# Optimization experiments

Measured on AMD Instinct MI355X. Metric: run time of the kernel, lower is better.

## Reference

```python
import jax, jax.numpy as jnp
import numpy as np

N_NODES = 50000
N_EDGES = 800000
F_IN = 64
F_HID = 64
F_OUT = 16


def setup_inputs() -> dict:
    key = jax.random.key(0)
    k1, k2, k3, k4, k5 = jax.random.split(key, 5)
    x = jax.random.normal(k1, (N_NODES, F_IN), dtype=jnp.float32)
    edge_index = jax.random.randint(k2, (2, N_EDGES), 0, N_NODES, dtype=jnp.int64)
    # glorot-style init for GCNConv weights
    W1 = jax.random.normal(k3, (F_IN, F_HID), dtype=jnp.float32) * (1.0 / np.sqrt(F_IN))
    b1 = jnp.zeros((F_HID,), dtype=jnp.float32)
    W2 = jax.random.normal(k4, (F_HID, F_OUT), dtype=jnp.float32) * (1.0 / np.sqrt(F_HID))
    b2 = jnp.zeros((F_OUT,), dtype=jnp.float32)
    return {"x": x, "edge_index": edge_index, "W1": W1, "b1": b1, "W2": W2, "b2": b2}


def _gcn_conv(x, src, dst, n, W, b):
    # linear transform first (PyG GCNConv), then normalized scatter-add aggregation
    h = x @ W  # [N, F_out]
    deg = jax.ops.segment_sum(jnp.ones_like(dst, dtype=h.dtype), dst, num_segments=n)
    dinv = jnp.where(deg > 0, jax.lax.rsqrt(deg), 0.0)  # deg^{-1/2}, 0 for isolated
    norm = dinv[src] * dinv[dst]  # [E]
    out = jax.ops.segment_sum(norm[:, None] * h[src], dst, num_segments=n)
    return out + b


def reference(x, edge_index, W1, b1, W2, b2):
    n = x.shape[0]
    loops = jnp.arange(n, dtype=edge_index.dtype)
    # add self-loops as in PyG GCNConv default
    src = jnp.concatenate([edge_index[0], loops])
    dst = jnp.concatenate([edge_index[1], loops])
    h = jax.nn.relu(_gcn_conv(x, src, dst, n, W1, b1))
    h = _gcn_conv(h, src, dst, n, W2, b2)
    return jax.nn.log_softmax(h, axis=1)
```

## Files before the change

### kernel.cpp

```cpp
#include <hip/hip_runtime.h>


#define F1 64
#define F2 16
#define G 256
#define HP 512

typedef __attribute__((ext_vector_type(8))) short bf16x8;
typedef __attribute__((ext_vector_type(4))) float f32x4;

__device__ inline void cvt8(const float* v, bf16x8& h, bf16x8& l) {
#pragma unroll
    for (int i = 0; i < 8; ++i) {
        unsigned b = __float_as_uint(v[i]);
        h[i] = (short)(b >> 16);
        float hif = __uint_as_float(b & 0xFFFF0000u);
        float lof = v[i] - hif;
        l[i] = (short)(__float_as_uint(lof) >> 16);
    }
}


__global__ __launch_bounds__(256) void k_hist(const int* __restrict__ dst,
                                              int* __restrict__ hist,
                                              int* __restrict__ ptotal,
                                              int e, int npart) {
    __shared__ int hl[HP];
    int tid = threadIdx.x, g = blockIdx.x;
    for (int i = tid; i < HP; i += 256) hl[i] = 0;
    __syncthreads();
    int chunk = (e + G - 1) / G;
    int beg = g * chunk, end = min(e, beg + chunk);
    for (int i = beg + tid; i < end; i += 256)
        atomicAdd(&hl[dst[i] >> 7], 1);
    __syncthreads();
    for (int p = tid; p < npart; p += 256) {
        int v = hl[p];
        hist[g * HP + p] = v;
        if (v) atomicAdd(&ptotal[p], v);
    }
}

__global__ __launch_bounds__(512) void k_pscan(const int* __restrict__ ptotal,
                                               int* __restrict__ part_base,
                                               int* __restrict__ rowstart,
                                               int npart, int n, int e) {
    __shared__ int s[512];
    int tid = threadIdx.x;
    int v = (tid < npart) ? ptotal[tid] : 0;
    s[tid] = v;
    __syncthreads();
    for (int off = 1; off < 512; off <<= 1) {
        int t = (tid >= off) ? s[tid - off] : 0;
        __syncthreads();
        s[tid] += t;
        __syncthreads();
    }
    if (tid < npart) part_base[tid] = s[tid] - v;
    if (tid == 0) { part_base[npart] = e; rowstart[n] = e; }
}

__global__ __launch_bounds__(256) void k_cscan(const int* __restrict__ hist,
                                               const int* __restrict__ part_base,
                                               int* __restrict__ pgoff, int npart) {
    __shared__ int s[G];
    int p = blockIdx.x, g = threadIdx.x;
    int v = hist[g * HP + p];
    s[g] = v;
    __syncthreads();
    for (int off = 1; off < G; off <<= 1) {
        int t = (g >= off) ? s[g - off] : 0;
        __syncthreads();
        s[g] += t;
        __syncthreads();
    }
    pgoff[g * HP + p] = part_base[p] + s[g] - v;
}

__global__ __launch_bounds__(256) void k_part(const int* __restrict__ src,
                                              const int* __restrict__ dst,
                                              const int* __restrict__ pgoff,
                                              unsigned* __restrict__ pairs,
                                              int e, int npart) {
    __shared__ int cur[HP];
    int tid = threadIdx.x, g = blockIdx.x;
    for (int i = tid; i < npart; i += 256) cur[i] = pgoff[g * HP + i];
    __syncthreads();
    int chunk = (e + G - 1) / G;
    int beg = g * chunk, end = min(e, beg + chunk);
    for (int i = beg + tid; i < end; i += 256) {
        int d = dst[i], sv = src[i];
        int pos = atomicAdd(&cur[d >> 7], 1);
        pairs[pos] = ((unsigned)(d & 127) << 16) | (unsigned)sv;
    }
}

__global__ __launch_bounds__(256) void k_csr(const unsigned* __restrict__ pairs,
                                             const int* __restrict__ part_base,
                                             int* __restrict__ rowstart,
                                             float* __restrict__ dinv,
                                             int* __restrict__ csr, int n) {
    __shared__ int cnt[128], cur[128], sc[128];
    int p = blockIdx.x, tid = threadIdx.x;
    int wbeg = part_base[p], wend = part_base[p + 1];
    if (tid < 128) cnt[tid] = 0;
    __syncthreads();
    for (int i = wbeg + tid; i < wend; i += 256)
        atomicAdd(&cnt[pairs[i] >> 16], 1);
    __syncthreads();
    if (tid < 128) sc[tid] = cnt[tid];
    __syncthreads();
    for (int off = 1; off < 128; off <<= 1) {
        int t = (tid >= off && tid < 128) ? sc[tid - off] : 0;
        __syncthreads();
        if (tid < 128) sc[tid] += t;
        __syncthreads();
    }
    if (tid < 128) {
        int v = cnt[tid];
        int rs = wbeg + sc[tid] - v;
        cur[tid] = rs;
        int node = (p << 7) + tid;
        if (node < n) {
            rowstart[node] = rs;
            dinv[node] = rsqrtf((float)v + 1.0f);
        }
    }
    __syncthreads();
    for (int i = wbeg + tid; i < wend; i += 256) {
        unsigned u = pairs[i];
        int pos = atomicAdd(&cur[u >> 16], 1);
        csr[pos] = (int)(u & 0xFFFFu);
    }
}


__global__ __launch_bounds__(256) void k_mgemm1(const float* __restrict__ x,
                                                const float* __restrict__ W1,
                                                float* __restrict__ h, int n) {
    __shared__ float ws[64 * 65];
    int tid = threadIdx.x;
    for (int i = tid; i < 64 * 64; i += 256) {
        int k = i >> 6, c = i & 63;
        ws[k * 65 + c] = W1[i];
    }
    __syncthreads();
    int lane = tid & 63, wv = tid >> 6;
    int rt = blockIdx.x * 64 + wv * 16;
    int r = lane & 15, g = lane >> 4;
    int row = rt + r;
    int rowc = row < n ? row : n - 1;
    const float* xp = x + (size_t)rowc * F1 + g * 8;
    bf16x8 ah[2], al[2];
#pragma unroll
    for (int kb = 0; kb < 2; ++kb) {
        float v[8];
        *(float4*)&v[0] = *(const float4*)(xp + kb * 32);
        *(float4*)&v[4] = *(const float4*)(xp + kb * 32 + 4);
        cvt8(v, ah[kb], al[kb]);
    }
#pragma unroll
    for (int ct = 0; ct < 4; ++ct) {
        bf16x8 bh[2], bl[2];
#pragma unroll
        for (int kb = 0; kb < 2; ++kb) {
            float v[8];
#pragma unroll
            for (int i = 0; i < 8; ++i)
                v[i] = ws[(kb * 32 + g * 8 + i) * 65 + ct * 16 + r];
            cvt8(v, bh[kb], bl[kb]);
        }
        f32x4 acc = {0.f, 0.f, 0.f, 0.f};
#pragma unroll
        for (int kb = 0; kb < 2; ++kb) {
            acc = __builtin_amdgcn_mfma_f32_16x16x32_bf16(ah[kb], bh[kb], acc, 0, 0, 0);
            acc = __builtin_amdgcn_mfma_f32_16x16x32_bf16(al[kb], bh[kb], acc, 0, 0, 0);
            acc = __builtin_amdgcn_mfma_f32_16x16x32_bf16(ah[kb], bl[kb], acc, 0, 0, 0);
        }
#pragma unroll
        for (int j = 0; j < 4; ++j) {
            int orow = rt + g * 4 + j;
            if (orow < n) h[(size_t)orow * F1 + ct * 16 + r] = acc[j];
        }
    }
}

__global__ __launch_bounds__(256) void k_mgemm2(const float* __restrict__ agg1,
                                                const float* __restrict__ b1,
                                                const float* __restrict__ W2,
                                                float* __restrict__ h2, int n) {
    __shared__ float ws[64 * 17];
    int tid = threadIdx.x;
    for (int i = tid; i < 64 * 16; i += 256) {
        int k = i >> 4, c = i & 15;
        ws[k * 17 + c] = W2[i];
    }
    __syncthreads();
    int lane = tid & 63, wv = tid >> 6;
    int rt = blockIdx.x * 64 + wv * 16;
    int r = lane & 15, g = lane >> 4;
    int row = rt + r;
    int rowc = row < n ? row : n - 1;
    const float* ap = agg1 + (size_t)rowc * F1 + g * 8;
    const float* bp = b1 + g * 8;
    bf16x8 ah[2], al[2];
#pragma unroll
    for (int kb = 0; kb < 2; ++kb) {
        float v[8], b[8];
        *(float4*)&v[0] = *(const float4*)(ap + kb * 32);
        *(float4*)&v[4] = *(const float4*)(ap + kb * 32 + 4);
        *(float4*)&b[0] = *(const float4*)(bp + kb * 32);
        *(float4*)&b[4] = *(const float4*)(bp + kb * 32 + 4);
#pragma unroll
        for (int i = 0; i < 8; ++i) v[i] = fmaxf(v[i] + b[i], 0.f);
        cvt8(v, ah[kb], al[kb]);
    }
    bf16x8 bh[2], bl[2];
#pragma unroll
    for (int kb = 0; kb < 2; ++kb) {
        float v[8];
#pragma unroll
        for (int i = 0; i < 8; ++i)
            v[i] = ws[(kb * 32 + g * 8 + i) * 17 + r];
        cvt8(v, bh[kb], bl[kb]);
    }
    f32x4 acc = {0.f, 0.f, 0.f, 0.f};
#pragma unroll
    for (int kb = 0; kb < 2; ++kb) {
        acc = __builtin_amdgcn_mfma_f32_16x16x32_bf16(ah[kb], bh[kb], acc, 0, 0, 0);
        acc = __builtin_amdgcn_mfma_f32_16x16x32_bf16(al[kb], bh[kb], acc, 0, 0, 0);
        acc = __builtin_amdgcn_mfma_f32_16x16x32_bf16(ah[kb], bl[kb], acc, 0, 0, 0);
    }
#pragma unroll
    for (int j = 0; j < 4; ++j) {
        int orow = rt + g * 4 + j;
        if (orow < n) h2[(size_t)orow * F2 + r] = acc[j];
    }
}


__global__ __launch_bounds__(256) void k_agg64(const int* __restrict__ rowstart,
                                               const int* __restrict__ csr,
                                               const float* __restrict__ dinv,
                                               const float* __restrict__ h,
                                               float* __restrict__ agg, int n) {
    int lane = threadIdx.x & 63, wv = threadIdx.x >> 6;
    int node = blockIdx.x * 4 + wv;
    if (node >= n) return;
    int g = lane >> 4, q = lane & 15;
    float di = dinv[node];
    const float4* h4 = (const float4*)h;
    float4 acc = {0.f, 0.f, 0.f, 0.f};
    int beg = rowstart[node], end = rowstart[node + 1];
    for (int base = beg; base < end; base += 64) {
        int k = base + lane;
        int idx = (k < end) ? csr[k] : 0;
        float dv = (k < end) ? dinv[idx] : 0.0f;
        int m = end - base;
        if (m > 64) m = 64;
        int iters = (m + 3) >> 2;
        for (int i = 0; i < iters; ++i) {
            int slot = i * 4 + g;
            int s = __shfl(idx, slot, 64);
            float w = __shfl(dv, slot, 64);
            float4 v = h4[(size_t)s * 16 + q];
            acc.x = fmaf(w, v.x, acc.x);
            acc.y = fmaf(w, v.y, acc.y);
            acc.z = fmaf(w, v.z, acc.z);
            acc.w = fmaf(w, v.w, acc.w);
        }
    }
#pragma unroll
    for (int off = 16; off <= 32; off <<= 1) {
        acc.x += __shfl_xor(acc.x, off, 64);
        acc.y += __shfl_xor(acc.y, off, 64);
        acc.z += __shfl_xor(acc.z, off, 64);
        acc.w += __shfl_xor(acc.w, off, 64);
    }
    if (g == 0) {
        float4 sv = h4[(size_t)node * 16 + q];
        float d2 = di * di;
        float4 o;
        o.x = fmaf(di, acc.x, d2 * sv.x);
        o.y = fmaf(di, acc.y, d2 * sv.y);
        o.z = fmaf(di, acc.z, d2 * sv.z);
        o.w = fmaf(di, acc.w, d2 * sv.w);
        ((float4*)agg)[(size_t)node * 16 + q] = o;
    }
}

__global__ __launch_bounds__(256) void k_agg16(const int* __restrict__ rowstart,
                                               const int* __restrict__ csr,
                                               const float* __restrict__ dinv,
                                               const float* __restrict__ h2,
                                               const float* __restrict__ b2,
                                               float* __restrict__ out, int n) {
    int lane = threadIdx.x & 63, wv = threadIdx.x >> 6;
    int node = blockIdx.x * 4 + wv;
    if (node >= n) return;
    int g = lane >> 2, q = lane & 3;
    float di = dinv[node];
    const float4* h4 = (const float4*)h2;
    float4 acc = {0.f, 0.f, 0.f, 0.f};
    int beg = rowstart[node], end = rowstart[node + 1];
    for (int base = beg; base < end; base += 64) {
        int k = base + lane;
        int idx = (k < end) ? csr[k] : 0;
        float dv = (k < end) ? dinv[idx] : 0.0f;
        int m = end - base;
        if (m > 64) m = 64;
        int iters = (m + 15) >> 4;
        for (int i = 0; i < iters; ++i) {
            int slot = i * 16 + g;
            int s = __shfl(idx, slot, 64);
            float w = __shfl(dv, slot, 64);
            float4 v = h4[(size_t)s * 4 + q];
            acc.x = fmaf(w, v.x, acc.x);
            acc.y = fmaf(w, v.y, acc.y);
            acc.z = fmaf(w, v.z, acc.z);
            acc.w = fmaf(w, v.w, acc.w);
        }
    }
#pragma unroll
    for (int off = 4; off <= 32; off <<= 1) {
        acc.x += __shfl_xor(acc.x, off, 64);
        acc.y += __shfl_xor(acc.y, off, 64);
        acc.z += __shfl_xor(acc.z, off, 64);
        acc.w += __shfl_xor(acc.w, off, 64);
    }
    float4 sv = h4[(size_t)node * 4 + q];
    float4 bv = ((const float4*)b2)[q];
    float d2 = di * di;
    float4 v;
    v.x = fmaf(di, acc.x, fmaf(d2, sv.x, bv.x));
    v.y = fmaf(di, acc.y, fmaf(d2, sv.y, bv.y));
    v.z = fmaf(di, acc.z, fmaf(d2, sv.z, bv.z));
    v.w = fmaf(di, acc.w, fmaf(d2, sv.w, bv.w));
    float mr = fmaxf(fmaxf(v.x, v.y), fmaxf(v.z, v.w));
    mr = fmaxf(mr, __shfl_xor(mr, 1, 64));
    mr = fmaxf(mr, __shfl_xor(mr, 2, 64));
    float s = expf(v.x - mr) + expf(v.y - mr) + expf(v.z - mr) + expf(v.w - mr);
    s += __shfl_xor(s, 1, 64);
    s += __shfl_xor(s, 2, 64);
    float l = mr + logf(s);
    if (g == 0) {
        float4 o;
        o.x = v.x - l; o.y = v.y - l; o.z = v.z - l; o.w = v.w - l;
        ((float4*)out)[(size_t)node * 4 + q] = o;
    }
}

extern "C" void kernel_launch(void* const* d_in, const int* in_sizes, int n_in,
                              void* d_out, int out_size, void* d_ws, size_t ws_size,
                              hipStream_t stream) {
    const float* x  = (const float*)d_in[0];
    const int*   ei = (const int*)d_in[1];
    const float* W1 = (const float*)d_in[2];
    const float* b1 = (const float*)d_in[3];
    const float* W2 = (const float*)d_in[4];
    const float* b2 = (const float*)d_in[5];
    float* out = (float*)d_out;

    const int n = in_sizes[0] / F1;
    const int e = in_sizes[1] / 2;
    const int* src = ei;
    const int* dst = ei + e;

    const int na = (n + 63) & ~63;
    const int npart = (n + 127) >> 7;

    float* dinv     = (float*)d_ws;
    int* rowstart   = (int*)(dinv + na);
    int* part_base  = rowstart + na + 64;
    int* ptotal     = part_base + 576;
    int* csr        = ptotal + 512;
    float* h        = (float*)(csr + ((e + 63) & ~63));
    float* agg1     = h + (size_t)n * F1;
    int* hist       = (int*)h;
    int* pgoff      = hist + G * HP;
    unsigned* pairs = (unsigned*)(pgoff + G * HP);

    hipMemsetAsync(ptotal, 0, HP * sizeof(int), stream);
    k_hist <<<G, 256, 0, stream>>>(dst, hist, ptotal, e, npart);
    k_pscan<<<1, 512, 0, stream>>>(ptotal, part_base, rowstart, npart, n, e);
    k_cscan<<<npart, 256, 0, stream>>>(hist, part_base, pgoff, npart);
    k_part <<<G, 256, 0, stream>>>(src, dst, pgoff, pairs, e, npart);
    k_csr  <<<npart, 256, 0, stream>>>(pairs, part_base, rowstart, dinv, csr, n);

    k_mgemm1<<<(n + 63) / 64, 256, 0, stream>>>(x, W1, h, n);
    k_agg64<<<(n + 3) / 4, 256, 0, stream>>>(rowstart, csr, dinv, h, agg1, n);

    float* h2 = h;
    k_mgemm2<<<(n + 63) / 64, 256, 0, stream>>>(agg1, b1, W2, h2, n);
    k_agg16<<<(n + 3) / 4, 256, 0, stream>>>(rowstart, csr, dinv, h2, b2, out, n);
}
```

Measured before the change: 171.2 us.

## Store GEMM outputs in bf16 and simplify CSR build to fewer kernels

Both GEMM stages now write their outputs as bf16 instead of fp32, halving the gather traffic in the two aggregation kernels. The CSR construction widens partitions to 256 nodes, drops the memset and the single-block prefix-scan kernel by recomputing partition bases redundantly in each block, and vectorises the edge reads with int4 loads. This removes two launches and some serial work, but the bf16 storage lowers the precision of the gathered features. Packing the source index into 16 bits assumes node ids fit that field (50000 does).

```diff
diff --git a/kernel.cpp b/kernel.cpp
--- a/kernel.cpp
+++ b/kernel.cpp
@@ -4,10 +4,19 @@
 #define F1 64
 #define F2 16
 #define G 256
-#define HP 512
+#define HP 256
 
 typedef __attribute__((ext_vector_type(8))) short bf16x8;
 typedef __attribute__((ext_vector_type(4))) float f32x4;
+typedef __attribute__((ext_vector_type(4))) unsigned short u16x4;
+
+__device__ inline unsigned short f2bf(float f) {
+    unsigned u = __float_as_uint(f);
+    return (unsigned short)((u + 0x7FFFu + ((u >> 16) & 1u)) >> 16);
+}
+__device__ inline float bf2f(unsigned short s) {
+    return __uint_as_float(((unsigned)s) << 16);
+}
 
 __device__ inline void cvt8(const float* v, bf16x8& h, bf16x8& l) {
 #pragma unroll
@@ -21,48 +30,31 @@
 }
 
 
-__global__ __launch_bounds__(256) void k_hist(const int* __restrict__ dst,
-                                              int* __restrict__ hist,
-                                              int* __restrict__ ptotal,
-                                              int e, int npart) {
+__global__ __launch_bounds__(256) void k_hist(const int4* __restrict__ dst4,
+                                              const int* __restrict__ dst,
+                                              int* __restrict__ hist, int e4, int e) {
     __shared__ int hl[HP];
     int tid = threadIdx.x, g = blockIdx.x;
-    for (int i = tid; i < HP; i += 256) hl[i] = 0;
-    __syncthreads();
-    int chunk = (e + G - 1) / G;
-    int beg = g * chunk, end = min(e, beg + chunk);
-    for (int i = beg + tid; i < end; i += 256)
-        atomicAdd(&hl[dst[i] >> 7], 1);
-    __syncthreads();
-    for (int p = tid; p < npart; p += 256) {
-        int v = hl[p];
-        hist[g * HP + p] = v;
-        if (v) atomicAdd(&ptotal[p], v);
-    }
-}
-
-__global__ __launch_bounds__(512) void k_pscan(const int* __restrict__ ptotal,
-                                               int* __restrict__ part_base,
-                                               int* __restrict__ rowstart,
-                                               int npart, int n, int e) {
-    __shared__ int s[512];
-    int tid = threadIdx.x;
-    int v = (tid < npart) ? ptotal[tid] : 0;
-    s[tid] = v;
-    __syncthreads();
-    for (int off = 1; off < 512; off <<= 1) {
-        int t = (tid >= off) ? s[tid - off] : 0;
-        __syncthreads();
-        s[tid] += t;
-        __syncthreads();
-    }
-    if (tid < npart) part_base[tid] = s[tid] - v;
-    if (tid == 0) { part_base[npart] = e; rowstart[n] = e; }
+    hl[tid] = 0;
+    __syncthreads();
+    int chunk = (e4 + G - 1) / G;
+    int beg = g * chunk, end = min(e4, beg + chunk);
+    for (int i = beg + tid; i < end; i += 256) {
+        int4 d = dst4[i];
+        atomicAdd(&hl[d.x >> 8], 1);
+        atomicAdd(&hl[d.y >> 8], 1);
+        atomicAdd(&hl[d.z >> 8], 1);
+        atomicAdd(&hl[d.w >> 8], 1);
+    }
+    if (g == G - 1)
+        for (int i = e4 * 4 + tid; i < e; i += 256) atomicAdd(&hl[dst[i] >> 8], 1);
+    __syncthreads();
+    hist[g * HP + tid] = hl[tid];
 }
 
 __global__ __launch_bounds__(256) void k_cscan(const int* __restrict__ hist,
-                                               const int* __restrict__ part_base,
-                                               int* __restrict__ pgoff, int npart) {
+                                               int* __restrict__ pgoff,
+                                               int* __restrict__ ptotal) {
     __shared__ int s[G];
     int p = blockIdx.x, g = threadIdx.x;
     int v = hist[g * HP + p];
@@ -74,58 +66,94 @@
         s[g] += t;
         __syncthreads();
     }
-    pgoff[g * HP + p] = part_base[p] + s[g] - v;
-}
-
-__global__ __launch_bounds__(256) void k_part(const int* __restrict__ src,
+    pgoff[g * HP + p] = s[g] - v;
+    if (g == G - 1) ptotal[p] = s[g];
+}
+
+__global__ __launch_bounds__(256) void k_part(const int4* __restrict__ src4,
+                                              const int4* __restrict__ dst4,
+                                              const int* __restrict__ src,
                                               const int* __restrict__ dst,
                                               const int* __restrict__ pgoff,
+                                              const int* __restrict__ ptotal,
                                               unsigned* __restrict__ pairs,
-                                              int e, int npart) {
+                                              int e4, int e, int npart) {
+    __shared__ int s[HP];
     __shared__ int cur[HP];
     int tid = threadIdx.x, g = blockIdx.x;
-    for (int i = tid; i < npart; i += 256) cur[i] = pgoff[g * HP + i];
-    __syncthreads();
-    int chunk = (e + G - 1) / G;
-    int beg = g * chunk, end = min(e, beg + chunk);
+    int v = (tid < npart) ? ptotal[tid] : 0;
+    s[tid] = v;
+    __syncthreads();
+    for (int off = 1; off < HP; off <<= 1) {
+        int t = (tid >= off) ? s[tid - off] : 0;
+        __syncthreads();
+        s[tid] += t;
+        __syncthreads();
+    }
+    cur[tid] = (s[tid] - v) + pgoff[g * HP + tid];
+    __syncthreads();
+    int chunk = (e4 + G - 1) / G;
+    int beg = g * chunk, end = min(e4, beg + chunk);
     for (int i = beg + tid; i < end; i += 256) {
-        int d = dst[i], sv = src[i];
-        int pos = atomicAdd(&cur[d >> 7], 1);
-        pairs[pos] = ((unsigned)(d & 127) << 16) | (unsigned)sv;
-    }
+        int4 s4 = src4[i];
+        int4 d4 = dst4[i];
+        int pos;
+        pos = atomicAdd(&cur[d4.x >> 8], 1); pairs[pos] = ((unsigned)(d4.x & 255) << 16) | (unsigned)s4.x;
+        pos = atomicAdd(&cur[d4.y >> 8], 1); pairs[pos] = ((unsigned)(d4.y & 255) << 16) | (unsigned)s4.y;
+        pos = atomicAdd(&cur[d4.z >> 8], 1); pairs[pos] = ((unsigned)(d4.z & 255) << 16) | (unsigned)s4.z;
+        pos = atomicAdd(&cur[d4.w >> 8], 1); pairs[pos] = ((unsigned)(d4.w & 255) << 16) | (unsigned)s4.w;
+    }
+    if (g == G - 1)
+        for (int i = e4 * 4 + tid; i < e; i += 256) {
+            int d = dst[i];
+            int pos = atomicAdd(&cur[d >> 8], 1);
+            pairs[pos] = ((unsigned)(d & 255) << 16) | (unsigned)src[i];
+        }
 }
 
 __global__ __launch_bounds__(256) void k_csr(const unsigned* __restrict__ pairs,
-                                             const int* __restrict__ part_base,
+                                             const int* __restrict__ ptotal,
                                              int* __restrict__ rowstart,
                                              float* __restrict__ dinv,
-                                             int* __restrict__ csr, int n) {
-    __shared__ int cnt[128], cur[128], sc[128];
+                                             int* __restrict__ csr,
+                                             int n, int e, int npart) {
+    __shared__ int s[HP];
+    __shared__ int cnt[256], cur[256];
+    __shared__ int wbs, wes;
     int p = blockIdx.x, tid = threadIdx.x;
-    int wbeg = part_base[p], wend = part_base[p + 1];
-    if (tid < 128) cnt[tid] = 0;
-    __syncthreads();
+    int v = (tid < npart) ? ptotal[tid] : 0;
+    s[tid] = v;
+    __syncthreads();
+    for (int off = 1; off < HP; off <<= 1) {
+        int t = (tid >= off) ? s[tid - off] : 0;
+        __syncthreads();
+        s[tid] += t;
+        __syncthreads();
+    }
+    if (tid == p) { wbs = s[tid] - v; wes = s[tid]; }
+    cnt[tid] = 0;
+    __syncthreads();
+    int wbeg = wbs, wend = wes;
     for (int i = wbeg + tid; i < wend; i += 256)
         atomicAdd(&cnt[pairs[i] >> 16], 1);
     __syncthreads();
-    if (tid < 128) sc[tid] = cnt[tid];
-    __syncthreads();
-    for (int off = 1; off < 128; off <<= 1) {
-        int t = (tid >= off && tid < 128) ? sc[tid - off] : 0;
-        __syncthreads();
-        if (tid < 128) sc[tid] += t;
-        __syncthreads();
-    }
-    if (tid < 128) {
-        int v = cnt[tid];
-        int rs = wbeg + sc[tid] - v;
-        cur[tid] = rs;
-        int node = (p << 7) + tid;
-        if (node < n) {
-            rowstart[node] = rs;
-            dinv[node] = rsqrtf((float)v + 1.0f);
-        }
-    }
+    int c = cnt[tid];
+    s[tid] = c;
+    __syncthreads();
+    for (int off = 1; off < 256; off <<= 1) {
+        int t = (tid >= off) ? s[tid - off] : 0;
+        __syncthreads();
+        s[tid] += t;
+        __syncthreads();
+    }
+    int rs = wbeg + s[tid] - c;
+    cur[tid] = rs;
+    int node = (p << 8) + tid;
+    if (node < n) {
+        rowstart[node] = rs;
+        dinv[node] = rsqrtf((float)c + 1.0f);
+    }
+    if (p == 0 && tid == 0) rowstart[n] = e;
     __syncthreads();
     for (int i = wbeg + tid; i < wend; i += 256) {
         unsigned u = pairs[i];
@@ -137,7 +165,7 @@
 
 __global__ __launch_bounds__(256) void k_mgemm1(const float* __restrict__ x,
                                                 const float* __restrict__ W1,
-                                                float* __restrict__ h, int n) {
+                                                unsigned short* __restrict__ h_bf, int n) {
     __shared__ float ws[64 * 65];
     int tid = threadIdx.x;
     for (int i = tid; i < 64 * 64; i += 256) {
@@ -180,7 +208,7 @@
 #pragma unroll
         for (int j = 0; j < 4; ++j) {
             int orow = rt + g * 4 + j;
-            if (orow < n) h[(size_t)orow * F1 + ct * 16 + r] = acc[j];
+            if (orow < n) h_bf[(size_t)orow * F1 + ct * 16 + r] = f2bf(acc[j]);
         }
     }
 }
@@ -188,7 +216,7 @@
 __global__ __launch_bounds__(256) void k_mgemm2(const float* __restrict__ agg1,
                                                 const float* __restrict__ b1,
                                                 const float* __restrict__ W2,
-                                                float* __restrict__ h2, int n) {
+                                                unsigned short* __restrict__ h2_bf, int n) {
     __shared__ float ws[64 * 17];
     int tid = threadIdx.x;
     for (int i = tid; i < 64 * 16; i += 256) {
@@ -234,7 +262,7 @@
 #pragma unroll
     for (int j = 0; j < 4; ++j) {
         int orow = rt + g * 4 + j;
-        if (orow < n) h2[(size_t)orow * F2 + r] = acc[j];
+        if (orow < n) h2_bf[(size_t)orow * F2 + r] = f2bf(acc[j]);
     }
 }
 
@@ -242,14 +270,13 @@
 __global__ __launch_bounds__(256) void k_agg64(const int* __restrict__ rowstart,
                                                const int* __restrict__ csr,
                                                const float* __restrict__ dinv,
-                                               const float* __restrict__ h,
+                                               const unsigned short* __restrict__ hb,
                                                float* __restrict__ agg, int n) {
     int lane = threadIdx.x & 63, wv = threadIdx.x >> 6;
     int node = blockIdx.x * 4 + wv;
     if (node >= n) return;
     int g = lane >> 4, q = lane & 15;
     float di = dinv[node];
-    const float4* h4 = (const float4*)h;
     float4 acc = {0.f, 0.f, 0.f, 0.f};
     int beg = rowstart[node], end = rowstart[node + 1];
     for (int base = beg; base < end; base += 64) {
@@ -263,11 +290,11 @@
             int slot = i * 4 + g;
             int s = __shfl(idx, slot, 64);
             float w = __shfl(dv, slot, 64);
-            float4 v = h4[(size_t)s * 16 + q];
-            acc.x = fmaf(w, v.x, acc.x);
-            acc.y = fmaf(w, v.y, acc.y);
-            acc.z = fmaf(w, v.z, acc.z);
-            acc.w = fmaf(w, v.w, acc.w);
+            u16x4 u = *(const u16x4*)(hb + (size_t)s * F1 + q * 4);
+            acc.x = fmaf(w, bf2f(u.x), acc.x);
+            acc.y = fmaf(w, bf2f(u.y), acc.y);
+            acc.z = fmaf(w, bf2f(u.z), acc.z);
+            acc.w = fmaf(w, bf2f(u.w), acc.w);
         }
     }
 #pragma unroll
@@ -278,13 +305,13 @@
         acc.w += __shfl_xor(acc.w, off, 64);
     }
     if (g == 0) {
-        float4 sv = h4[(size_t)node * 16 + q];
+        u16x4 su = *(const u16x4*)(hb + (size_t)node * F1 + q * 4);
         float d2 = di * di;
         float4 o;
-        o.x = fmaf(di, acc.x, d2 * sv.x);
-        o.y = fmaf(di, acc.y, d2 * sv.y);
-        o.z = fmaf(di, acc.z, d2 * sv.z);
-        o.w = fmaf(di, acc.w, d2 * sv.w);
+        o.x = fmaf(di, acc.x, d2 * bf2f(su.x));
+        o.y = fmaf(di, acc.y, d2 * bf2f(su.y));
+        o.z = fmaf(di, acc.z, d2 * bf2f(su.z));
+        o.w = fmaf(di, acc.w, d2 * bf2f(su.w));
         ((float4*)agg)[(size_t)node * 16 + q] = o;
     }
 }
@@ -292,7 +319,7 @@
 __global__ __launch_bounds__(256) void k_agg16(const int* __restrict__ rowstart,
                                                const int* __restrict__ csr,
                                                const float* __restrict__ dinv,
-                                               const float* __restrict__ h2,
+                                               const unsigned short* __restrict__ h2b,
                                                const float* __restrict__ b2,
                                                float* __restrict__ out, int n) {
     int lane = threadIdx.x & 63, wv = threadIdx.x >> 6;
@@ -300,7 +327,6 @@
     if (node >= n) return;
     int g = lane >> 2, q = lane & 3;
     float di = dinv[node];
-    const float4* h4 = (const float4*)h2;
     float4 acc = {0.f, 0.f, 0.f, 0.f};
     int beg = rowstart[node], end = rowstart[node + 1];
     for (int base = beg; base < end; base += 64) {
@@ -314,11 +340,11 @@
             int slot = i * 16 + g;
             int s = __shfl(idx, slot, 64);
             float w = __shfl(dv, slot, 64);
-            float4 v = h4[(size_t)s * 4 + q];
-            acc.x = fmaf(w, v.x, acc.x);
-            acc.y = fmaf(w, v.y, acc.y);
-            acc.z = fmaf(w, v.z, acc.z);
-            acc.w = fmaf(w, v.w, acc.w);
+            u16x4 u = *(const u16x4*)(h2b + (size_t)s * F2 + q * 4);
+            acc.x = fmaf(w, bf2f(u.x), acc.x);
+            acc.y = fmaf(w, bf2f(u.y), acc.y);
+            acc.z = fmaf(w, bf2f(u.z), acc.z);
+            acc.w = fmaf(w, bf2f(u.w), acc.w);
         }
     }
 #pragma unroll
@@ -328,21 +354,21 @@
         acc.z += __shfl_xor(acc.z, off, 64);
         acc.w += __shfl_xor(acc.w, off, 64);
     }
-    float4 sv = h4[(size_t)node * 4 + q];
+    u16x4 su = *(const u16x4*)(h2b + (size_t)node * F2 + q * 4);
     float4 bv = ((const float4*)b2)[q];
     float d2 = di * di;
     float4 v;
-    v.x = fmaf(di, acc.x, fmaf(d2, sv.x, bv.x));
-    v.y = fmaf(di, acc.y, fmaf(d2, sv.y, bv.y));
-    v.z = fmaf(di, acc.z, fmaf(d2, sv.z, bv.z));
-    v.w = fmaf(di, acc.w, fmaf(d2, sv.w, bv.w));
+    v.x = fmaf(di, acc.x, fmaf(d2, bf2f(su.x), bv.x));
+    v.y = fmaf(di, acc.y, fmaf(d2, bf2f(su.y), bv.y));
+    v.z = fmaf(di, acc.z, fmaf(d2, bf2f(su.z), bv.z));
+    v.w = fmaf(di, acc.w, fmaf(d2, bf2f(su.w), bv.w));
     float mr = fmaxf(fmaxf(v.x, v.y), fmaxf(v.z, v.w));
     mr = fmaxf(mr, __shfl_xor(mr, 1, 64));
     mr = fmaxf(mr, __shfl_xor(mr, 2, 64));
-    float s = expf(v.x - mr) + expf(v.y - mr) + expf(v.z - mr) + expf(v.w - mr);
-    s += __shfl_xor(s, 1, 64);
-    s += __shfl_xor(s, 2, 64);
-    float l = mr + logf(s);
+    float sm = expf(v.x - mr) + expf(v.y - mr) + expf(v.z - mr) + expf(v.w - mr);
+    sm += __shfl_xor(sm, 1, 64);
+    sm += __shfl_xor(sm, 2, 64);
+    float l = mr + logf(sm);
     if (g == 0) {
         float4 o;
         o.x = v.x - l; o.y = v.y - l; o.z = v.z - l; o.w = v.w - l;
@@ -363,34 +389,33 @@
 
     const int n = in_sizes[0] / F1;
     const int e = in_sizes[1] / 2;
+    const int e4 = e >> 2;
     const int* src = ei;
     const int* dst = ei + e;
 
     const int na = (n + 63) & ~63;
-    const int npart = (n + 127) >> 7;
+    const int npart = (n + 255) >> 8;
 
     float* dinv     = (float*)d_ws;
     int* rowstart   = (int*)(dinv + na);
-    int* part_base  = rowstart + na + 64;
-    int* ptotal     = part_base + 576;
-    int* csr        = ptotal + 512;
-    float* h        = (float*)(csr + ((e + 63) & ~63));
-    float* agg1     = h + (size_t)n * F1;
-    int* hist       = (int*)h;
+    int* ptotal     = rowstart + na + 64;
+    int* csr        = ptotal + 256;
+    unsigned short* h_bf = (unsigned short*)(csr + ((e + 63) & ~63));
+    float* agg1     = (float*)(h_bf + (size_t)n * F1);
+    int* hist       = (int*)h_bf;
     int* pgoff      = hist + G * HP;
     unsigned* pairs = (unsigned*)(pgoff + G * HP);
-
-    hipMemsetAsync(ptotal, 0, HP * sizeof(int), stream);
-    k_hist <<<G, 256, 0, stream>>>(dst, hist, ptotal, e, npart);
-    k_pscan<<<1, 512, 0, stream>>>(ptotal, part_base, rowstart, npart, n, e);
-    k_cscan<<<npart, 256, 0, stream>>>(hist, part_base, pgoff, npart);
-    k_part <<<G, 256, 0, stream>>>(src, dst, pgoff, pairs, e, npart);
-    k_csr  <<<npart, 256, 0, stream>>>(pairs, part_base, rowstart, dinv, csr, n);
-
-    k_mgemm1<<<(n + 63) / 64, 256, 0, stream>>>(x, W1, h, n);
-    k_agg64<<<(n + 3) / 4, 256, 0, stream>>>(rowstart, csr, dinv, h, agg1, n);
-
-    float* h2 = h;
-    k_mgemm2<<<(n + 63) / 64, 256, 0, stream>>>(agg1, b1, W2, h2, n);
-    k_agg16<<<(n + 3) / 4, 256, 0, stream>>>(rowstart, csr, dinv, h2, b2, out, n);
-}
+    unsigned short* h2_bf = h_bf;
+
+    k_hist <<<G, 256, 0, stream>>>((const int4*)dst, dst, hist, e4, e);
+    k_cscan<<<npart, 256, 0, stream>>>(hist, pgoff, ptotal);
+    k_part <<<G, 256, 0, stream>>>((const int4*)src, (const int4*)dst, src, dst,
+                                   pgoff, ptotal, pairs, e4, e, npart);
+    k_csr  <<<npart, 256, 0, stream>>>(pairs, ptotal, rowstart, dinv, csr, n, e, npart);
+
+    k_mgemm1<<<(n + 63) / 64, 256, 0, stream>>>(x, W1, h_bf, n);
+    k_agg64<<<(n + 3) / 4, 256, 0, stream>>>(rowstart, csr, dinv, h_bf, agg1, n);
+
+    k_mgemm2<<<(n + 63) / 64, 256, 0, stream>>>(agg1, b1, W2, h2_bf, n);
+    k_agg16<<<(n + 3) / 4, 256, 0, stream>>>(rowstart, csr, dinv, h2_bf, b2, out, n);
+}
```

New measurement: 158.5 us. 1.08x faster.
